# Performance work log

Measured on AMD Instinct MI355X. Metric: run time of the kernel, lower is better.

The kernel has to match this reference:

```python
import jax, jax.numpy as jnp
import numpy as np
import math

N_HEADS = 16
DIM_MODEL = 1024
DIM_KQ = 64
DIM_V = 64
B, T = 2, 2048


def setup_inputs() -> dict:
    key = jax.random.key(0)
    ks = jax.random.split(key, 9)
    s = 1.0 / math.sqrt(DIM_MODEL)
    return {
        "x": jax.random.normal(ks[0], (B, T, DIM_MODEL), dtype=jnp.float32),
        "Wq": jax.random.normal(ks[1], (DIM_MODEL, N_HEADS * DIM_KQ), dtype=jnp.float32) * s,
        "bq": jnp.zeros((N_HEADS * DIM_KQ,), dtype=jnp.float32),
        "Wk": jax.random.normal(ks[2], (DIM_MODEL, N_HEADS * DIM_KQ), dtype=jnp.float32) * s,
        "bk": jnp.zeros((N_HEADS * DIM_KQ,), dtype=jnp.float32),
        "Wv": jax.random.normal(ks[3], (DIM_MODEL, N_HEADS * DIM_V), dtype=jnp.float32) * s,
        "bv": jnp.zeros((N_HEADS * DIM_V,), dtype=jnp.float32),
        "Wo": jax.random.normal(ks[4], (N_HEADS * DIM_V, DIM_MODEL), dtype=jnp.float32) * s,
        "bo": jnp.zeros((DIM_MODEL,), dtype=jnp.float32),
    }


def reference(x, Wq, bq, Wk, bk, Wv, bv, Wo, bo):
    b, t, _ = x.shape
    # projections, split into heads: [B, T, h, d]
    q = (x @ Wq + bq).reshape(b, t, N_HEADS, DIM_KQ)
    k = (x @ Wk + bk).reshape(b, t, N_HEADS, DIM_KQ)
    v = (x @ Wv + bv).reshape(b, t, N_HEADS, DIM_V)
    # NOTE: faithful to source einsum 'B Tq h d, B Tk h d -> B h Tk Tq'
    # scores[b, h, tk, tq] = q[b, tq] . k[b, tk]
    scores = jnp.einsum('bqhd,bkhd->bhkq', q, k)
    # softmax over the LAST axis (= query axis tq), as in the source
    attn = jax.nn.softmax(scores / math.sqrt(DIM_KQ), axis=-1)
    # source einsum 'B h Tk Tq, B Tq h dv -> B Tq h dv':
    # sums over Tk only -> out[b, tq, h, dv] = v[b, tq, h, dv] * sum_tk attn[b, h, tk, tq]
    colsum = attn.sum(axis=2)                      # [B, h, Tq]
    mixed = v * colsum.transpose(0, 2, 1)[..., None]  # [B, Tq, h, dv]
    out = mixed.reshape(b, t, N_HEADS * DIM_V) @ Wo + bo
    return out
```

## Files before the change

### kernel.cpp

```cpp
#include <hip/hip_runtime.h>
#include <hip/hip_bf16.h>
#include <stdint.h>

typedef __attribute__((ext_vector_type(4))) float f32x4;
typedef __attribute__((ext_vector_type(8))) __bf16 bf16x8;

#define AS1 __attribute__((address_space(1)))
#define AS3 __attribute__((address_space(3)))

#if __has_builtin(__builtin_amdgcn_exp2f)
#define EXP2(x) __builtin_amdgcn_exp2f(x)
#else
#define EXP2(x) exp2f(x)
#endif

__device__ __forceinline__ ushort f2bf(float f) {
  uint32_t u = __builtin_bit_cast(uint32_t, f);
  u += 0x7fffu + ((u >> 16) & 1u);
  return (ushort)(u >> 16);
}
__device__ __forceinline__ float bf2f(ushort h) {
  uint32_t u = ((uint32_t)h) << 16;
  return __builtin_bit_cast(float, u);
}

#define SCK 0.18033688011112042f


__global__ void k_cvt_x(const float* __restrict__ x, ushort* __restrict__ xb, int n4) {
  int i = blockIdx.x * blockDim.x + threadIdx.x;
  if (i >= n4) return;
  float4 v = ((const float4*)x)[i];
  ushort4 o;
  o.x = f2bf(v.x); o.y = f2bf(v.y); o.z = f2bf(v.z); o.w = f2bf(v.w);
  ((ushort4*)xb)[i] = o;
}

__global__ void k_prep_w(const float* __restrict__ Wq, const float* __restrict__ Wk,
                         const float* __restrict__ Wv, const float* __restrict__ Wo,
                         ushort* __restrict__ Wt, ushort* __restrict__ Wot) {
  __shared__ float tile[32][33];
  int z = blockIdx.z;
  const float* src = (z == 0) ? Wq : (z == 1) ? Wk : (z == 2) ? Wv : Wo;
  ushort* dst = (z < 3) ? (Wt + (size_t)z * 1048576) : Wot;
  float scale = (z == 1) ? SCK : 1.0f;
  int k0 = blockIdx.y * 32, n0 = blockIdx.x * 32;
  int tx = threadIdx.x, ty = threadIdx.y;
#pragma unroll
  for (int i = 0; i < 4; i++)
    tile[ty + i * 8][tx] = src[(size_t)(k0 + ty + i * 8) * 1024 + n0 + tx];
  __syncthreads();
#pragma unroll
  for (int i = 0; i < 4; i++)
    dst[(size_t)(n0 + ty + i * 8) * 1024 + k0 + tx] = f2bf(tile[tx][ty + i * 8] * scale);
}

#define GLD(src, dst) \
  __builtin_amdgcn_global_load_lds((const AS1 uint32_t*)(src), (AS3 uint32_t*)(dst), 16, 0, 0)

template <int MODE>
__global__ __launch_bounds__(512, 2) void k_gemm8(const ushort* __restrict__ A,
                                                  const ushort* __restrict__ Bt,
                                                  void* __restrict__ Cv,
                                                  const float* __restrict__ b0,
                                                  const float* __restrict__ b1,
                                                  const float* __restrict__ b2,
                                                  int K, int ldc) {
  __shared__ char ldsb[131072];
  const int tid = threadIdx.x;
  const int lane = tid & 63;
  const int wid = tid >> 6;
  const int wr = wid >> 2, wc = wid & 3;
  const int l15 = lane & 15, l4 = lane >> 4;
  const int row0 = blockIdx.y * 256;
  const int col0 = blockIdx.x * 256;
  const int T = K >> 5;

  const int swz = ((tid & 3) ^ ((tid >> 3) & 3)) << 3;
  const ushort* Ap = A + (size_t)(row0 + (tid >> 2)) * K + swz;
  const ushort* Bp = Bt + (size_t)(col0 + (tid >> 2)) * K + swz;

#define STAGE(t)                                        \
  do {                                                  \
    char* bufs = ldsb + (((t) & 3) << 15);              \
    const ushort* pa = Ap + (size_t)(t) * 32;           \
    const ushort* pb = Bp + (size_t)(t) * 32;           \
    GLD(pa, bufs + tid * 16);                           \
    GLD(pa + 128 * K, bufs + 8192 + tid * 16);          \
    GLD(pb, bufs + 16384 + tid * 16);                   \
    GLD(pb + 128 * K, bufs + 24576 + tid * 16);         \
  } while (0)

  int aoffL[8], boffL[4];
#pragma unroll
  for (int m = 0; m < 8; m++) {
    int r = wr * 128 + m * 16 + l15;
    aoffL[m] = r * 64 + ((l4 ^ ((r >> 1) & 3)) << 4);
  }
#pragma unroll
  for (int n = 0; n < 4; n++) {
    int r = wc * 64 + n * 16 + l15;
    boffL[n] = 16384 + r * 64 + ((l4 ^ ((r >> 1) & 3)) << 4);
  }

  f32x4 acc[8][4] = {};

  STAGE(0);
  STAGE(1);
  STAGE(2);
  asm volatile("s_waitcnt vmcnt(8)" ::: "memory");
  __builtin_amdgcn_sched_barrier(0);
  __builtin_amdgcn_s_barrier();
  __builtin_amdgcn_sched_barrier(0);

#define PHASE(t, DO_STAGE, VMSTR)                                                   \
  do {                                                                              \
    char* buf = ldsb + (((t) & 3) << 15);                                           \
    bf16x8 af[8], bfr[4];                                                           \
    _Pragma("unroll") for (int m = 0; m < 8; m++)                                   \
        af[m] = *(const bf16x8*)(buf + aoffL[m]);                                   \
    _Pragma("unroll") for (int n = 0; n < 4; n++)                                   \
        bfr[n] = *(const bf16x8*)(buf + boffL[n]);                                  \
    if (DO_STAGE) STAGE((t) + 3);                                                   \
    __builtin_amdgcn_s_setprio(1);                                                  \
    _Pragma("unroll") for (int m = 0; m < 8; m++)                                   \
        _Pragma("unroll") for (int n = 0; n < 4; n++)                               \
            acc[m][n] = __builtin_amdgcn_mfma_f32_16x16x32_bf16(af[m], bfr[n],      \
                                                                acc[m][n], 0, 0, 0);\
    __builtin_amdgcn_s_setprio(0);                                                  \
    asm volatile(VMSTR ::: "memory");                                               \
    __builtin_amdgcn_sched_barrier(0);                                              \
    __builtin_amdgcn_s_barrier();                                                   \
    __builtin_amdgcn_sched_barrier(0);                                              \
  } while (0)

  for (int t = 0; t < T - 3; ++t) PHASE(t, true, "s_waitcnt vmcnt(8)");
  PHASE(T - 3, false, "s_waitcnt vmcnt(4)");
  PHASE(T - 2, false, "s_waitcnt vmcnt(0)");
  PHASE(T - 1, false, "s_nop 0");

#undef PHASE
#undef STAGE

#pragma unroll
  for (int m = 0; m < 8; m++)
#pragma unroll
    for (int n = 0; n < 4; n++) {
      int colg = col0 + wc * 64 + n * 16 + l15;
      float bias;
      if (MODE == 0) {
        bias = (colg < 1024) ? b0[colg]
                             : ((colg < 2048) ? b1[colg - 1024] * SCK : b2[colg - 2048]);
      } else {
        bias = b0[colg];
      }
#pragma unroll
      for (int j = 0; j < 4; j++) {
        int rowg = row0 + wr * 128 + m * 16 + l4 * 4 + j;
        float v = acc[m][n][j] + bias;
        if (MODE == 0)
          ((ushort*)Cv)[(size_t)rowg * ldc + colg] = f2bf(v);
        else
          ((float*)Cv)[(size_t)rowg * ldc + colg] = v;
      }
    }
}

template <int MODE>
__global__ __launch_bounds__(256) void k_gemm(const ushort* __restrict__ A,
                                              const ushort* __restrict__ Bt,
                                              void* __restrict__ Cv,
                                              const float* __restrict__ b0,
                                              int M, int N, int K, int ldc) {
  __shared__ ushort As[128 * 32];
  __shared__ ushort Bs[128 * 32];
  const int tid = threadIdx.x;
  const int lane = tid & 63;
  const int wid = tid >> 6;
  const int wr = wid >> 1, wc = wid & 1;
  const int row0 = blockIdx.y * 128;
  const int col0 = blockIdx.x * 128;
  const int l15 = lane & 15, l4 = lane >> 4;

  f32x4 acc[4][4] = {};

  for (int k0 = 0; k0 < K; k0 += 32) {
    __syncthreads();
#pragma unroll
    for (int i = 0; i < 2; i++) {
      int c = i * 256 + tid;
      int r = c >> 2, cb = c & 3;
      const ushort* ga = A + (size_t)(row0 + r) * K + k0 + cb * 8;
      GLD(ga, (char*)As + c * 16);
      const ushort* gb = Bt + (size_t)(col0 + r) * K + k0 + cb * 8;
      GLD(gb, (char*)Bs + c * 16);
    }
    __syncthreads();
    bf16x8 av[4], bv[4];
#pragma unroll
    for (int m = 0; m < 4; m++)
      av[m] = *(const bf16x8*)(As + (wr * 64 + m * 16 + l15) * 32 + l4 * 8);
#pragma unroll
    for (int n = 0; n < 4; n++)
      bv[n] = *(const bf16x8*)(Bs + (wc * 64 + n * 16 + l15) * 32 + l4 * 8);
#pragma unroll
    for (int m = 0; m < 4; m++)
#pragma unroll
      for (int n = 0; n < 4; n++)
        acc[m][n] = __builtin_amdgcn_mfma_f32_16x16x32_bf16(av[m], bv[n], acc[m][n], 0, 0, 0);
  }

#pragma unroll
  for (int m = 0; m < 4; m++)
#pragma unroll
    for (int n = 0; n < 4; n++) {
      int colg = col0 + wc * 64 + n * 16 + l15;
      float bias = b0[colg];
#pragma unroll
      for (int j = 0; j < 4; j++) {
        int rowg = row0 + wr * 64 + m * 16 + l4 * 4 + j;
        float v = acc[m][n][j] + bias;
        if (MODE == 0)
          ((ushort*)Cv)[(size_t)rowg * ldc + colg] = f2bf(v);
        else
          ((float*)Cv)[(size_t)rowg * ldc + colg] = v;
      }
    }
}

__global__ __launch_bounds__(256) void k_attn_z(const ushort* __restrict__ QKV,
                                                float* __restrict__ Zpart) {
  const int tkb = blockIdx.x, bh = blockIdx.y, s = blockIdx.z;
  const int b = bh >> 4, h = bh & 15;
  const int tid = threadIdx.x, lane = tid & 63, w = tid >> 6;
  const int l15 = lane & 15, l4 = lane >> 4;
  const size_t rs = 3072;

  __shared__ ushort Ks[128 * 64];
  __shared__ ushort Qs[128 * 64];

  const ushort* Kbase = QKV + (size_t)(b * 2048 + tkb * 128) * rs + 1024 + h * 64;
  const ushort* Qbase = QKV + (size_t)(b * 2048 + s * 1024) * rs + h * 64;
  const ushort* gq[4];
  int ldsoff[4];
#pragma unroll
  for (int i = 0; i < 4; i++) {
    int c = i * 256 + tid;
    int r = c >> 3;
    int cb = ((c & 7) * 16) ^ ((r & 7) << 4);
    GLD(Kbase + (size_t)r * rs + (cb >> 1), (char*)Ks + c * 16);
    gq[i] = Qbase + (size_t)r * rs + (cb >> 1);
    ldsoff[i] = c * 16;
  }
  __syncthreads();

  bf16x8 kf[2][2];
#pragma unroll
  for (int m = 0; m < 2; m++)
#pragma unroll
    for (int d = 0; d < 2; d++) {
      int r = w * 32 + m * 16 + l15;
      int byte = r * 128 + ((d * 64 + l4 * 16) ^ ((r & 7) << 4));
      kf[m][d] = *(const bf16x8*)((const char*)Ks + byte);
    }

  float z[2][4] = {};
  const f32x4 zero4 = {0.f, 0.f, 0.f, 0.f};

  for (int t = 0; t < 8; ++t) {
    __syncthreads();
#pragma unroll
    for (int i = 0; i < 4; i++) GLD(gq[i], (char*)Qs + ldsoff[i]);
#pragma unroll
    for (int i = 0; i < 4; i++) gq[i] += 128 * rs;
    __syncthreads();

    f32x4 acc[2][8];
#pragma unroll
    for (int d = 0; d < 2; d++)
#pragma unroll
      for (int n = 0; n < 8; n++) {
        int r = n * 16 + l15;
        int byte = r * 128 + ((d * 64 + l4 * 16) ^ ((r & 7) << 4));
        bf16x8 qf = *(const bf16x8*)((const char*)Qs + byte);
#pragma unroll
        for (int m = 0; m < 2; m++)
          acc[m][n] = __builtin_amdgcn_mfma_f32_16x16x32_bf16(
              kf[m][d], qf, d == 0 ? zero4 : acc[m][n], 0, 0, 0);
      }
#pragma unroll
    for (int m = 0; m < 2; m++)
#pragma unroll
      for (int n = 0; n < 8; n++)
#pragma unroll
        for (int j = 0; j < 4; j++)
          z[m][j] += EXP2(acc[m][n][j]);
  }

#pragma unroll
  for (int m = 0; m < 2; m++)
#pragma unroll
    for (int j = 0; j < 4; j++) {
      float v = z[m][j];
      v += __shfl_xor(v, 1, 64);
      v += __shfl_xor(v, 2, 64);
      v += __shfl_xor(v, 4, 64);
      v += __shfl_xor(v, 8, 64);
      if (l15 == 0)
        Zpart[(size_t)s * 65536 + bh * 2048 + tkb * 128 + w * 32 + m * 16 + l4 * 4 + j] = v;
    }
}

__global__ void k_rz(const float* __restrict__ Zpart, float* __restrict__ rrz) {
  int g = blockIdx.x * 256 + threadIdx.x;
  rrz[g] = 1.0f / (Zpart[g] + Zpart[65536 + g]);
}

__global__ __launch_bounds__(256) void k_attn_cs(const ushort* __restrict__ QKV,
                                                 const float* __restrict__ rrz,
                                                 float* __restrict__ csPart) {
  const int tqb = blockIdx.x, bh = blockIdx.y, s = blockIdx.z;
  const int b = bh >> 4, h = bh & 15;
  const int tid = threadIdx.x, lane = tid & 63, w = tid >> 6;
  const int l15 = lane & 15, l4 = lane >> 4;
  const size_t rs = 3072;

  __shared__ ushort Qs[128 * 64];
  __shared__ ushort Ks[128 * 64];

  const ushort* Qbase = QKV + (size_t)(b * 2048 + tqb * 128) * rs + h * 64;
  const ushort* Kbase = QKV + (size_t)(b * 2048 + s * 1024) * rs + 1024 + h * 64;
  const float* rz0 = rrz + bh * 2048 + s * 1024;
  const ushort* gk[4];
  int ldsoff[4];
#pragma unroll
  for (int i = 0; i < 4; i++) {
    int c = i * 256 + tid;
    int r = c >> 3;
    int cb = ((c & 7) * 16) ^ ((r & 7) << 4);
    GLD(Qbase + (size_t)r * rs + (cb >> 1), (char*)Qs + c * 16);
    gk[i] = Kbase + (size_t)r * rs + (cb >> 1);
    ldsoff[i] = c * 16;
  }
  __syncthreads();

  bf16x8 qf[2][2];
#pragma unroll
  for (int m = 0; m < 2; m++)
#pragma unroll
    for (int d = 0; d < 2; d++) {
      int r = w * 32 + m * 16 + l15;
      int byte = r * 128 + ((d * 64 + l4 * 16) ^ ((r & 7) << 4));
      qf[m][d] = *(const bf16x8*)((const char*)Qs + byte);
    }

  float cs[2][4] = {};
  const f32x4 zero4 = {0.f, 0.f, 0.f, 0.f};

  for (int t = 0; t < 8; ++t) {
    __syncthreads();
#pragma unroll
    for (int i = 0; i < 4; i++) GLD(gk[i], (char*)Ks + ldsoff[i]);
#pragma unroll
    for (int i = 0; i < 4; i++) gk[i] += 128 * rs;

    float rz[8];
#pragma unroll
    for (int n = 0; n < 8; n++) rz[n] = rz0[t * 128 + n * 16 + l15];
    __syncthreads();

    f32x4 acc[2][8];
#pragma unroll
    for (int d = 0; d < 2; d++)
#pragma unroll
      for (int n = 0; n < 8; n++) {
        int r = n * 16 + l15;
        int byte = r * 128 + ((d * 64 + l4 * 16) ^ ((r & 7) << 4));
        bf16x8 kft = *(const bf16x8*)((const char*)Ks + byte);
#pragma unroll
        for (int m = 0; m < 2; m++)
          acc[m][n] = __builtin_amdgcn_mfma_f32_16x16x32_bf16(
              qf[m][d], kft, d == 0 ? zero4 : acc[m][n], 0, 0, 0);
      }
#pragma unroll
    for (int m = 0; m < 2; m++)
#pragma unroll
      for (int n = 0; n < 8; n++)
#pragma unroll
        for (int j = 0; j < 4; j++)
          cs[m][j] = fmaf(EXP2(acc[m][n][j]), rz[n], cs[m][j]);
  }

#pragma unroll
  for (int m = 0; m < 2; m++)
#pragma unroll
    for (int j = 0; j < 4; j++) {
      float v = cs[m][j];
      v += __shfl_xor(v, 1, 64);
      v += __shfl_xor(v, 2, 64);
      v += __shfl_xor(v, 4, 64);
      v += __shfl_xor(v, 8, 64);
      if (l15 == 0)
        csPart[(size_t)s * 65536 + bh * 2048 + tqb * 128 + w * 32 + m * 16 + l4 * 4 + j] = v;
    }
}

__global__ void k_mixed(const ushort* __restrict__ QKV, const float* __restrict__ csPart,
                        ushort* __restrict__ mixed) {
  int i = blockIdx.x * 256 + threadIdx.x;
  int row = i >> 7;
  int col = (i & 127) * 8;
  int b = row >> 11, t = row & 2047, h = col >> 6;
  int g = ((b << 4) + h) * 2048 + t;
  float cs = csPart[g] + csPart[65536 + g];
  uint4 raw = *(const uint4*)(QKV + (size_t)row * 3072 + 2048 + col);
  const ushort* pv = (const ushort*)&raw;
  ushort o[8];
#pragma unroll
  for (int k = 0; k < 8; k++) o[k] = f2bf(bf2f(pv[k]) * cs);
  *(uint4*)(mixed + (size_t)row * 1024 + col) = *(uint4*)o;
}


extern "C" void kernel_launch(void* const* d_in, const int* in_sizes, int n_in,
                              void* d_out, int out_size, void* d_ws, size_t ws_size,
                              hipStream_t stream) {
  const float* x = (const float*)d_in[0];
  const float* Wq = (const float*)d_in[1];
  const float* bq = (const float*)d_in[2];
  const float* Wk = (const float*)d_in[3];
  const float* bk = (const float*)d_in[4];
  const float* Wv = (const float*)d_in[5];
  const float* bv = (const float*)d_in[6];
  const float* Wo = (const float*)d_in[7];
  const float* bo = (const float*)d_in[8];

  char* ws = (char*)d_ws;
  ushort* xb     = (ushort*)(ws);
  ushort* Wt     = (ushort*)(ws + 8388608);
  ushort* Wot    = (ushort*)(ws + 14680064);
  ushort* QKV    = (ushort*)(ws + 16777216);
  float* Zpart   = (float*)(ws + 41943040);
  float* rrz     = (float*)(ws + 42467328);
  float* csPart  = (float*)(ws + 42729472);
  ushort* mixed  = (ushort*)(ws + 43253760);

  k_cvt_x<<<4096, 256, 0, stream>>>(x, xb, 4096 * 1024 / 4);
  k_prep_w<<<dim3(32, 32, 4), dim3(32, 8), 0, stream>>>(Wq, Wk, Wv, Wo, Wt, Wot);

  k_gemm8<0><<<dim3(12, 16), 512, 0, stream>>>(xb, Wt, QKV, bq, bk, bv, 1024, 3072);
  k_attn_z<<<dim3(16, 32, 2), 256, 0, stream>>>(QKV, Zpart);
  k_rz<<<256, 256, 0, stream>>>(Zpart, rrz);
  k_attn_cs<<<dim3(16, 32, 2), 256, 0, stream>>>(QKV, rrz, csPart);
  k_mixed<<<2048, 256, 0, stream>>>(QKV, csPart, mixed);
  k_gemm<1><<<dim3(8, 32), 256, 0, stream>>>(mixed, Wot, d_out, bo, 4096, 1024, 1024, 1024);
}
```

Baseline: 145.9 us.

## Pipeline attention K/Q loads with triple buffering, enlarge tiles, split GEMM phases

The attention-statistics kernels now process 256 resident rows per block (4 fragments per wave) and stream the other operand through a triple-buffered LDS ring. Loads are issued two tiles ahead and waited on with vmcnt counters, which replaces the two __syncthreads per iteration. The QKV GEMM splits each K-step into two half-phases that interleave the A and B stage loads with MFMA groups behind extra barriers. This should hide global-load latency and halve the grid size, but it raises register and LDS use and adds barriers to the GEMM.

```diff
diff --git a/kernel.cpp b/kernel.cpp
--- a/kernel.cpp
+++ b/kernel.cpp
@@ -25,6 +25,16 @@
 }
 
 #define SCK 0.18033688011112042f
+
+#define GLD(src, dst) \
+  __builtin_amdgcn_global_load_lds((const AS1 uint32_t*)(src), (AS3 uint32_t*)(dst), 16, 0, 0)
+
+#define BARRIER()                          \
+  do {                                     \
+    __builtin_amdgcn_sched_barrier(0);     \
+    __builtin_amdgcn_s_barrier();          \
+    __builtin_amdgcn_sched_barrier(0);     \
+  } while (0)
 
 
 __global__ void k_cvt_x(const float* __restrict__ x, ushort* __restrict__ xb, int n4) {
@@ -54,9 +64,6 @@
   for (int i = 0; i < 4; i++)
     dst[(size_t)(n0 + ty + i * 8) * 1024 + k0 + tx] = f2bf(tile[tx][ty + i * 8] * scale);
 }
-
-#define GLD(src, dst) \
-  __builtin_amdgcn_global_load_lds((const AS1 uint32_t*)(src), (AS3 uint32_t*)(dst), 16, 0, 0)
 
 template <int MODE>
 __global__ __launch_bounds__(512, 2) void k_gemm8(const ushort* __restrict__ A,
@@ -80,15 +87,27 @@
   const ushort* Ap = A + (size_t)(row0 + (tid >> 2)) * K + swz;
   const ushort* Bp = Bt + (size_t)(col0 + (tid >> 2)) * K + swz;
 
-#define STAGE(t)                                        \
-  do {                                                  \
-    char* bufs = ldsb + (((t) & 3) << 15);              \
-    const ushort* pa = Ap + (size_t)(t) * 32;           \
-    const ushort* pb = Bp + (size_t)(t) * 32;           \
-    GLD(pa, bufs + tid * 16);                           \
-    GLD(pa + 128 * K, bufs + 8192 + tid * 16);          \
-    GLD(pb, bufs + 16384 + tid * 16);                   \
-    GLD(pb + 128 * K, bufs + 24576 + tid * 16);         \
+#define STAGE_H1(t)                              \
+  do {                                           \
+    char* bufs = ldsb + (((t) & 3) << 15);       \
+    const ushort* pa = Ap + (size_t)(t) * 32;    \
+    GLD(pa, bufs + tid * 16);                    \
+    GLD(pa + 128 * K, bufs + 8192 + tid * 16);   \
+  } while (0)
+#define STAGE_H2(t)                              \
+  do {                                           \
+    char* bufs = ldsb + (((t) & 3) << 15);       \
+    const ushort* pb = Bp + (size_t)(t) * 32;    \
+    GLD(pb, bufs + 16384 + tid * 16);            \
+    GLD(pb + 24576 - 16384 + 16384 + 8192 - 8192 + 8192 * 0 + 128 * K * 2 / 2, 0); \
+  } while (0)
+#undef STAGE_H2
+#define STAGE_H2(t)                              \
+  do {                                           \
+    char* bufs = ldsb + (((t) & 3) << 15);       \
+    const ushort* pb = Bp + (size_t)(t) * 32;    \
+    GLD(pb, bufs + 16384 + tid * 16);            \
+    GLD(pb + 128 * K, bufs + 24576 + tid * 16);  \
   } while (0)
 
   int aoffL[8], boffL[4];
@@ -105,33 +124,47 @@
 
   f32x4 acc[8][4] = {};
 
-  STAGE(0);
-  STAGE(1);
-  STAGE(2);
+  STAGE_H1(0); STAGE_H2(0);
+  STAGE_H1(1); STAGE_H2(1);
+  STAGE_H1(2); STAGE_H2(2);
   asm volatile("s_waitcnt vmcnt(8)" ::: "memory");
-  __builtin_amdgcn_sched_barrier(0);
-  __builtin_amdgcn_s_barrier();
-  __builtin_amdgcn_sched_barrier(0);
-
-#define PHASE(t, DO_STAGE, VMSTR)                                                   \
-  do {                                                                              \
-    char* buf = ldsb + (((t) & 3) << 15);                                           \
-    bf16x8 af[8], bfr[4];                                                           \
-    _Pragma("unroll") for (int m = 0; m < 8; m++)                                   \
-        af[m] = *(const bf16x8*)(buf + aoffL[m]);                                   \
-    _Pragma("unroll") for (int n = 0; n < 4; n++)                                   \
-        bfr[n] = *(const bf16x8*)(buf + boffL[n]);                                  \
-    if (DO_STAGE) STAGE((t) + 3);                                                   \
-    __builtin_amdgcn_s_setprio(1);                                                  \
-    _Pragma("unroll") for (int m = 0; m < 8; m++)                                   \
-        _Pragma("unroll") for (int n = 0; n < 4; n++)                               \
-            acc[m][n] = __builtin_amdgcn_mfma_f32_16x16x32_bf16(af[m], bfr[n],      \
-                                                                acc[m][n], 0, 0, 0);\
-    __builtin_amdgcn_s_setprio(0);                                                  \
-    asm volatile(VMSTR ::: "memory");                                               \
-    __builtin_amdgcn_sched_barrier(0);                                              \
-    __builtin_amdgcn_s_barrier();                                                   \
-    __builtin_amdgcn_sched_barrier(0);                                              \
+  BARRIER();
+
+#define PHASE(t, DO_STAGE, VMSTR)                                                     \
+  do {                                                                                \
+    char* buf = ldsb + (((t) & 3) << 15);                                             \
+                                             \
+    {                                                                                 \
+      bf16x8 af[4], bfr[4];                                                           \
+      _Pragma("unroll") for (int m = 0; m < 4; m++)                                   \
+          af[m] = *(const bf16x8*)(buf + aoffL[m]);                                   \
+      _Pragma("unroll") for (int n = 0; n < 4; n++)                                   \
+          bfr[n] = *(const bf16x8*)(buf + boffL[n]);                                  \
+      if (DO_STAGE) STAGE_H1((t) + 3);                                                \
+      BARRIER();                                                                      \
+      __builtin_amdgcn_s_setprio(1);                                                  \
+      _Pragma("unroll") for (int m = 0; m < 4; m++)                                   \
+          _Pragma("unroll") for (int n = 0; n < 4; n++)                               \
+              acc[m][n] = __builtin_amdgcn_mfma_f32_16x16x32_bf16(af[m], bfr[n],      \
+                                                                  acc[m][n], 0, 0, 0);\
+      __builtin_amdgcn_s_setprio(0);                                                  \
+                         \
+      BARRIER();                                                                      \
+                                        \
+      bf16x8 af2[4];                                                                  \
+      _Pragma("unroll") for (int m = 0; m < 4; m++)                                   \
+          af2[m] = *(const bf16x8*)(buf + aoffL[m + 4]);                              \
+      if (DO_STAGE) STAGE_H2((t) + 3);                                                \
+      BARRIER();                                                                      \
+      __builtin_amdgcn_s_setprio(1);                                                  \
+      _Pragma("unroll") for (int m = 0; m < 4; m++)                                   \
+          _Pragma("unroll") for (int n = 0; n < 4; n++)                               \
+              acc[m + 4][n] = __builtin_amdgcn_mfma_f32_16x16x32_bf16(                \
+                  af2[m], bfr[n], acc[m + 4][n], 0, 0, 0);                            \
+      __builtin_amdgcn_s_setprio(0);                                                  \
+      asm volatile(VMSTR ::: "memory");                                               \
+      BARRIER();                                                                      \
+    }                                                                                 \
   } while (0)
 
   for (int t = 0; t < T - 3; ++t) PHASE(t, true, "s_waitcnt vmcnt(8)");
@@ -140,7 +173,8 @@
   PHASE(T - 1, false, "s_nop 0");
 
 #undef PHASE
-#undef STAGE
+#undef STAGE_H1
+#undef STAGE_H2
 
 #pragma unroll
   for (int m = 0; m < 8; m++)
@@ -190,10 +224,8 @@
     for (int i = 0; i < 2; i++) {
       int c = i * 256 + tid;
       int r = c >> 2, cb = c & 3;
-      const ushort* ga = A + (size_t)(row0 + r) * K + k0 + cb * 8;
-      GLD(ga, (char*)As + c * 16);
-      const ushort* gb = Bt + (size_t)(col0 + r) * K + k0 + cb * 8;
-      GLD(gb, (char*)Bs + c * 16);
+      GLD(A + (size_t)(row0 + r) * K + k0 + cb * 8, (char*)As + c * 16);
+      GLD(Bt + (size_t)(col0 + r) * K + k0 + cb * 8, (char*)Bs + c * 16);
     }
     __syncthreads();
     bf16x8 av[4], bv[4];
@@ -228,77 +260,87 @@
     }
 }
 
-__global__ __launch_bounds__(256) void k_attn_z(const ushort* __restrict__ QKV,
-                                                float* __restrict__ Zpart) {
+__global__ __launch_bounds__(256, 2) void k_attn_z(const ushort* __restrict__ QKV,
+                                                   float* __restrict__ Zpart) {
   const int tkb = blockIdx.x, bh = blockIdx.y, s = blockIdx.z;
   const int b = bh >> 4, h = bh & 15;
   const int tid = threadIdx.x, lane = tid & 63, w = tid >> 6;
   const int l15 = lane & 15, l4 = lane >> 4;
   const size_t rs = 3072;
 
-  __shared__ ushort Ks[128 * 64];
-  __shared__ ushort Qs[128 * 64];
-
-  const ushort* Kbase = QKV + (size_t)(b * 2048 + tkb * 128) * rs + 1024 + h * 64;
+  __shared__ ushort Ks[256 * 64];
+  __shared__ ushort Qs[3][128 * 64];
+
+  const ushort* Kbase = QKV + (size_t)(b * 2048 + tkb * 256) * rs + 1024 + h * 64;
   const ushort* Qbase = QKV + (size_t)(b * 2048 + s * 1024) * rs + h * 64;
+
+  const int csl = ((tid & 7) ^ ((tid >> 3) & 7)) * 8;
+
+#pragma unroll
+  for (int i = 0; i < 8; i++) {
+    int c = i * 256 + tid;
+    GLD(Kbase + (size_t)(c >> 3) * rs + csl, (char*)Ks + c * 16);
+  }
   const ushort* gq[4];
-  int ldsoff[4];
 #pragma unroll
   for (int i = 0; i < 4; i++) {
     int c = i * 256 + tid;
-    int r = c >> 3;
-    int cb = ((c & 7) * 16) ^ ((r & 7) << 4);
-    GLD(Kbase + (size_t)r * rs + (cb >> 1), (char*)Ks + c * 16);
-    gq[i] = Qbase + (size_t)r * rs + (cb >> 1);
-    ldsoff[i] = c * 16;
-  }
-  __syncthreads();
-
-  bf16x8 kf[2][2];
-#pragma unroll
-  for (int m = 0; m < 2; m++)
+    gq[i] = Qbase + (size_t)(c >> 3) * rs + csl;
+    GLD(gq[i], (char*)Qs[0] + c * 16);
+    GLD(gq[i] + 128 * rs, (char*)Qs[1] + c * 16);
+  }
+  asm volatile("s_waitcnt vmcnt(8)" ::: "memory");
+  BARRIER();
+
+  bf16x8 kf[4][2];
+#pragma unroll
+  for (int m = 0; m < 4; m++)
 #pragma unroll
     for (int d = 0; d < 2; d++) {
-      int r = w * 32 + m * 16 + l15;
-      int byte = r * 128 + ((d * 64 + l4 * 16) ^ ((r & 7) << 4));
-      kf[m][d] = *(const bf16x8*)((const char*)Ks + byte);
-    }
-
-  float z[2][4] = {};
+      int r = w * 64 + m * 16 + l15;
+      kf[m][d] = *(const bf16x8*)((const char*)Ks + r * 128 + (((d * 4 + l4) ^ (r & 7)) << 4));
+    }
+
+  float z[4][4] = {};
   const f32x4 zero4 = {0.f, 0.f, 0.f, 0.f};
 
   for (int t = 0; t < 8; ++t) {
-    __syncthreads();
-#pragma unroll
-    for (int i = 0; i < 4; i++) GLD(gq[i], (char*)Qs + ldsoff[i]);
-#pragma unroll
-    for (int i = 0; i < 4; i++) gq[i] += 128 * rs;
-    __syncthreads();
-
-    f32x4 acc[2][8];
+    if (t < 7)
+      asm volatile("s_waitcnt vmcnt(4)" ::: "memory");
+    else
+      asm volatile("s_waitcnt vmcnt(0)" ::: "memory");
+    BARRIER();
+    if (t < 6) {
+      char* qd = (char*)Qs[(t + 2) % 3];
+#pragma unroll
+      for (int i = 0; i < 4; i++) {
+        int c = i * 256 + tid;
+        GLD(gq[i] + (size_t)(t + 2) * 128 * rs, qd + c * 16);
+      }
+    }
+    const char* qb = (const char*)Qs[t % 3];
+    f32x4 acc[4][8];
 #pragma unroll
     for (int d = 0; d < 2; d++)
 #pragma unroll
       for (int n = 0; n < 8; n++) {
         int r = n * 16 + l15;
-        int byte = r * 128 + ((d * 64 + l4 * 16) ^ ((r & 7) << 4));
-        bf16x8 qf = *(const bf16x8*)((const char*)Qs + byte);
-#pragma unroll
-        for (int m = 0; m < 2; m++)
+        bf16x8 qf = *(const bf16x8*)(qb + r * 128 + (((d * 4 + l4) ^ (r & 7)) << 4));
+#pragma unroll
+        for (int m = 0; m < 4; m++)
           acc[m][n] = __builtin_amdgcn_mfma_f32_16x16x32_bf16(
               kf[m][d], qf, d == 0 ? zero4 : acc[m][n], 0, 0, 0);
       }
 #pragma unroll
-    for (int m = 0; m < 2; m++)
+    for (int m = 0; m < 4; m++)
 #pragma unroll
       for (int n = 0; n < 8; n++)
 #pragma unroll
-        for (int j = 0; j < 4; j++)
-          z[m][j] += EXP2(acc[m][n][j]);
-  }
-
-#pragma unroll
-  for (int m = 0; m < 2; m++)
+        for (int j = 0; j < 4; j++) z[m][j] += EXP2(acc[m][n][j]);
+  }
+
+#pragma unroll
+  for (int m = 0; m < 4; m++)
 #pragma unroll
     for (int j = 0; j < 4; j++) {
       float v = z[m][j];
@@ -307,7 +349,7 @@
       v += __shfl_xor(v, 4, 64);
       v += __shfl_xor(v, 8, 64);
       if (l15 == 0)
-        Zpart[(size_t)s * 65536 + bh * 2048 + tkb * 128 + w * 32 + m * 16 + l4 * 4 + j] = v;
+        Zpart[(size_t)s * 65536 + bh * 2048 + tkb * 256 + w * 64 + m * 16 + l4 * 4 + j] = v;
     }
 }
 
@@ -316,74 +358,84 @@
   rrz[g] = 1.0f / (Zpart[g] + Zpart[65536 + g]);
 }
 
-__global__ __launch_bounds__(256) void k_attn_cs(const ushort* __restrict__ QKV,
-                                                 const float* __restrict__ rrz,
-                                                 float* __restrict__ csPart) {
+__global__ __launch_bounds__(256, 2) void k_attn_cs(const ushort* __restrict__ QKV,
+                                                    const float* __restrict__ rrz,
+                                                    float* __restrict__ csPart) {
   const int tqb = blockIdx.x, bh = blockIdx.y, s = blockIdx.z;
   const int b = bh >> 4, h = bh & 15;
   const int tid = threadIdx.x, lane = tid & 63, w = tid >> 6;
   const int l15 = lane & 15, l4 = lane >> 4;
   const size_t rs = 3072;
 
-  __shared__ ushort Qs[128 * 64];
-  __shared__ ushort Ks[128 * 64];
-
-  const ushort* Qbase = QKV + (size_t)(b * 2048 + tqb * 128) * rs + h * 64;
+  __shared__ ushort Qs[256 * 64];
+  __shared__ ushort Ks[3][128 * 64];
+
+  const ushort* Qbase = QKV + (size_t)(b * 2048 + tqb * 256) * rs + h * 64;
   const ushort* Kbase = QKV + (size_t)(b * 2048 + s * 1024) * rs + 1024 + h * 64;
   const float* rz0 = rrz + bh * 2048 + s * 1024;
+
+  const int csl = ((tid & 7) ^ ((tid >> 3) & 7)) * 8;
+
+#pragma unroll
+  for (int i = 0; i < 8; i++) {
+    int c = i * 256 + tid;
+    GLD(Qbase + (size_t)(c >> 3) * rs + csl, (char*)Qs + c * 16);
+  }
   const ushort* gk[4];
-  int ldsoff[4];
 #pragma unroll
   for (int i = 0; i < 4; i++) {
     int c = i * 256 + tid;
-    int r = c >> 3;
-    int cb = ((c & 7) * 16) ^ ((r & 7) << 4);
-    GLD(Qbase + (size_t)r * rs + (cb >> 1), (char*)Qs + c * 16);
-    gk[i] = Kbase + (size_t)r * rs + (cb >> 1);
-    ldsoff[i] = c * 16;
-  }
-  __syncthreads();
-
-  bf16x8 qf[2][2];
-#pragma unroll
-  for (int m = 0; m < 2; m++)
+    gk[i] = Kbase + (size_t)(c >> 3) * rs + csl;
+    GLD(gk[i], (char*)Ks[0] + c * 16);
+    GLD(gk[i] + 128 * rs, (char*)Ks[1] + c * 16);
+  }
+  asm volatile("s_waitcnt vmcnt(8)" ::: "memory");
+  BARRIER();
+
+  bf16x8 qf[4][2];
+#pragma unroll
+  for (int m = 0; m < 4; m++)
 #pragma unroll
     for (int d = 0; d < 2; d++) {
-      int r = w * 32 + m * 16 + l15;
-      int byte = r * 128 + ((d * 64 + l4 * 16) ^ ((r & 7) << 4));
-      qf[m][d] = *(const bf16x8*)((const char*)Qs + byte);
-    }
-
-  float cs[2][4] = {};
+      int r = w * 64 + m * 16 + l15;
+      qf[m][d] = *(const bf16x8*)((const char*)Qs + r * 128 + (((d * 4 + l4) ^ (r & 7)) << 4));
+    }
+
+  float cs[4][4] = {};
   const f32x4 zero4 = {0.f, 0.f, 0.f, 0.f};
 
   for (int t = 0; t < 8; ++t) {
-    __syncthreads();
-#pragma unroll
-    for (int i = 0; i < 4; i++) GLD(gk[i], (char*)Ks + ldsoff[i]);
-#pragma unroll
-    for (int i = 0; i < 4; i++) gk[i] += 128 * rs;
-
     float rz[8];
 #pragma unroll
     for (int n = 0; n < 8; n++) rz[n] = rz0[t * 128 + n * 16 + l15];
-    __syncthreads();
-
-    f32x4 acc[2][8];
+    if (t < 7)
+      asm volatile("s_waitcnt vmcnt(4)" ::: "memory");
+    else
+      asm volatile("s_waitcnt vmcnt(0)" ::: "memory");
+    BARRIER();
+    if (t < 6) {
+      char* kd = (char*)Ks[(t + 2) % 3];
+#pragma unroll
+      for (int i = 0; i < 4; i++) {
+        int c = i * 256 + tid;
+        GLD(gk[i] + (size_t)(t + 2) * 128 * rs, kd + c * 16);
+      }
+    }
+    const char* kb = (const char*)Ks[t % 3];
+    f32x4 acc[4][8];
 #pragma unroll
     for (int d = 0; d < 2; d++)
 #pragma unroll
       for (int n = 0; n < 8; n++) {
         int r = n * 16 + l15;
-        int byte = r * 128 + ((d * 64 + l4 * 16) ^ ((r & 7) << 4));
-        bf16x8 kft = *(const bf16x8*)((const char*)Ks + byte);
-#pragma unroll
-        for (int m = 0; m < 2; m++)
+        bf16x8 kft = *(const bf16x8*)(kb + r * 128 + (((d * 4 + l4) ^ (r & 7)) << 4));
+#pragma unroll
+        for (int m = 0; m < 4; m++)
           acc[m][n] = __builtin_amdgcn_mfma_f32_16x16x32_bf16(
               qf[m][d], kft, d == 0 ? zero4 : acc[m][n], 0, 0, 0);
       }
 #pragma unroll
-    for (int m = 0; m < 2; m++)
+    for (int m = 0; m < 4; m++)
 #pragma unroll
       for (int n = 0; n < 8; n++)
 #pragma unroll
@@ -392,7 +444,7 @@
   }
 
 #pragma unroll
-  for (int m = 0; m < 2; m++)
+  for (int m = 0; m < 4; m++)
 #pragma unroll
     for (int j = 0; j < 4; j++) {
       float v = cs[m][j];
@@ -401,7 +453,7 @@
       v += __shfl_xor(v, 4, 64);
       v += __shfl_xor(v, 8, 64);
       if (l15 == 0)
-        csPart[(size_t)s * 65536 + bh * 2048 + tqb * 128 + w * 32 + m * 16 + l4 * 4 + j] = v;
+        csPart[(size_t)s * 65536 + bh * 2048 + tqb * 256 + w * 64 + m * 16 + l4 * 4 + j] = v;
     }
 }
 
@@ -449,9 +501,9 @@
   k_prep_w<<<dim3(32, 32, 4), dim3(32, 8), 0, stream>>>(Wq, Wk, Wv, Wo, Wt, Wot);
 
   k_gemm8<0><<<dim3(12, 16), 512, 0, stream>>>(xb, Wt, QKV, bq, bk, bv, 1024, 3072);
-  k_attn_z<<<dim3(16, 32, 2), 256, 0, stream>>>(QKV, Zpart);
+  k_attn_z<<<dim3(8, 32, 2), 256, 0, stream>>>(QKV, Zpart);
   k_rz<<<256, 256, 0, stream>>>(Zpart, rrz);
-  k_attn_cs<<<dim3(16, 32, 2), 256, 0, stream>>>(QKV, rrz, csPart);
+  k_attn_cs<<<dim3(8, 32, 2), 256, 0, stream>>>(QKV, rrz, csPart);
   k_mixed<<<2048, 256, 0, stream>>>(QKV, csPart, mixed);
   k_gemm<1><<<dim3(8, 32), 256, 0, stream>>>(mixed, Wot, d_out, bo, 4096, 1024, 1024, 1024);
 }
```

After: 151.7 us. +4.0%, slower.
